# Performance work log

Hardware: AMD Instinct MI355X
Metric: run time of the kernel (lower is better)

Reference implementation:

```python
import jax, jax.numpy as jnp
import numpy as np

A = 64    # number of discrete actions (expert matrices)
D = 512   # input/output feature dim
B = 2048  # batch size


def setup_inputs() -> dict:
    key = jax.random.key(0)
    kx, ka, kw, kb = jax.random.split(key, 4)
    stdv = 1.0 / np.sqrt(D)  # matches torch init: uniform(-stdv, stdv), stdv = 1/sqrt(weight.size(1))
    x = jax.random.normal(kx, (B, D), dtype=jnp.float32)
    a = jax.random.randint(ka, (B,), 0, A, dtype=jnp.int64)
    weight = jax.random.uniform(kw, (A, D, D), dtype=jnp.float32, minval=-stdv, maxval=stdv)
    bias = jax.random.uniform(kb, (A, D), dtype=jnp.float32, minval=-stdv, maxval=stdv)
    return {"x": x, "a": a, "weight": weight, "bias": bias}


def reference(x, a, weight, bias):
    # Per-sample weight gather + batched matvec:
    #   z[b, i] = sum_j weight[a[b], i, j] * x[b, j] + bias[a[b], i]
    w = weight[a]                              # [B, D, D] gathered per-sample matrices
    z = jnp.einsum('bij,bj->bi', w, x)         # batched matvec
    z = z + bias[a]                            # per-sample bias gather + add
    return z
```

## Files before the change

### kernel.cpp

```cpp
#include <hip/hip_runtime.h>


#define NA 64
#define DD 512
#define NB 2048
#define BN 128
#define NW 8
#define BK 64
#define NSTEPS 8

typedef __bf16  bf16x8  __attribute__((ext_vector_type(8)));
typedef __bf16  bf16x4  __attribute__((ext_vector_type(4)));
typedef float   floatx4 __attribute__((ext_vector_type(4)));

#define GLD16(g, l)                                                         \
  __builtin_amdgcn_global_load_lds(                                         \
      (const __attribute__((address_space(1))) void*)(g),                   \
      (__attribute__((address_space(3))) void*)(l), 16, 0, 0)
#define VMCNT(n) asm volatile("s_waitcnt vmcnt(" #n ")" ::: "memory")
#define LGKMCNT0 asm volatile("s_waitcnt lgkmcnt(0)" ::: "memory")
#define SBAR     __builtin_amdgcn_s_barrier()
#define SCHED0   __builtin_amdgcn_sched_barrier(0)

static __device__ inline bf16x8 cvt8(floatx4 lo, floatx4 hi) {
    bf16x8 r;
    r[0] = (__bf16)lo[0]; r[1] = (__bf16)lo[1];
    r[2] = (__bf16)lo[2]; r[3] = (__bf16)lo[3];
    r[4] = (__bf16)hi[0]; r[5] = (__bf16)hi[1];
    r[6] = (__bf16)hi[2]; r[7] = (__bf16)hi[3];
    return r;
}

__global__ __launch_bounds__(512, 1) void dl_fused(
        const float* __restrict__ x,
        const int*   __restrict__ act,
        const float* __restrict__ weight,
        const float* __restrict__ bias,
        float*       __restrict__ out)
{
    const int a    = blockIdx.x;
    const int tid  = threadIdx.x;
    const int wave = tid >> 6;
    const int lane = tid & 63;
    const int l16  = lane & 15;
    const int kgrp = lane >> 4;
    const int colbase = blockIdx.y * BN;
    const int ncol    = colbase + wave * 16 + l16;

    __shared__ int s_perm[NB];
    __shared__ int s_wcnt[NW];
    __shared__ __align__(16) __bf16 Xs[64][DD];
    __shared__ __align__(16) float  Wl[2][BN][BK];

    const float* wtile = weight + (size_t)a * DD * DD + (size_t)colbase * DD;

    const int rr4 = lane >> 4;
    const int u16 = lane & 15;

    auto issue_step = [&](int slot, int s) {
#pragma unroll
        for (int c = 0; c < 4; ++c) {
            const int riw = c * 4 + rr4;
            GLD16(wtile + (size_t)(wave * 16 + riw) * DD + s * BK
                        + ((u16 ^ riw) << 2),
                  (char*)&Wl[slot][wave * 16 + c * 4][0]);
        }
    };

    const int ibase = wave * (NB / NW);
    int myact[NB / NW / 64];
#pragma unroll
    for (int it = 0; it < NB / NW / 64; ++it)
        myact[it] = act[ibase + it * 64 + lane];

    issue_step(0, 0);
    issue_step(1, 1);

    int wcnt = 0;
#pragma unroll
    for (int it = 0; it < NB / NW / 64; ++it) {
        unsigned long long m = __ballot(myact[it] == a);
        wcnt += (int)__popcll(m);
    }
    if (lane == 0) s_wcnt[wave] = wcnt;
    LGKMCNT0; SBAR;
    int cnt = 0, off = 0;
#pragma unroll
    for (int v = 0; v < NW; ++v) {
        const int c = s_wcnt[v];
        if (v < wave) off += c;
        cnt += c;
    }
    if (cnt == 0) { VMCNT(0); return; }
#pragma unroll
    for (int it = 0; it < NB / NW / 64; ++it) {
        unsigned long long m = __ballot(myact[it] == a);
        if (myact[it] == a) {
            int pos = off + (int)__popcll(m & ((1ull << lane) - 1ull));
            s_perm[pos] = ibase + it * 64 + lane;
        }
        off += (int)__popcll(m);
    }
    LGKMCNT0; SBAR;

    const float bias_v = bias[(size_t)a * DD + ncol];
    const int   h      = l16 & 7;
    const int   srow   = tid >> 5;
    const int   skk    = (tid & 31) << 2;

    for (int m0 = 0; m0 < cnt; m0 += 64) {
        if (m0 > 0) { issue_step(0, 0); issue_step(1, 1); }
        const int rem    = min(cnt - m0, 64);
        const int nchunk = (rem + 15) >> 4;

        floatx4 xv[16];
#pragma unroll
        for (int i = 0; i < 4; ++i) {
            const int r  = srow + 16 * i;
            const int rr = (r < rem) ? r : (rem - 1);
            const float* xr = x + (size_t)s_perm[m0 + rr] * DD;
#pragma unroll
            for (int j = 0; j < 4; ++j)
                xv[i * 4 + j] = *(const floatx4*)(xr + skk + 128 * j);
        }

#pragma unroll
        for (int i = 0; i < 4; ++i) {
            const int r = srow + 16 * i;
            if (r < rem) {
                const int rs = (r & 7) << 3;
#pragma unroll
                for (int j = 0; j < 4; ++j) {
                    const int f0 = skk + 128 * j;
                    bf16x4 bv;
#pragma unroll
                    for (int q = 0; q < 4; ++q) bv[q] = (__bf16)xv[i * 4 + j][q];
                    *(bf16x4*)&Xs[r][f0 ^ rs] = bv;
                }
            }
        }
        LGKMCNT0; SBAR;

        floatx4 acc[4] = {{0,0,0,0},{0,0,0,0},{0,0,0,0},{0,0,0,0}};
        const char* wlrow0 = (const char*)&Wl[0][wave * 16 + l16][0];
        const char* wlrow1 = (const char*)&Wl[1][wave * 16 + l16][0];

        auto compute = [&](int slot, int s) {
            const char* wl = slot ? wlrow1 : wlrow0;
#pragma unroll
            for (int s2 = 0; s2 < 2; ++s2) {
                const int u0 = s2 * 8 + kgrp * 2;
                const floatx4 blo = *(const floatx4*)(wl + (((u0)     ^ l16) << 4));
                const floatx4 bhi = *(const floatx4*)(wl + (((u0 + 1) ^ l16) << 4));
                const bf16x8 bfrag = cvt8(blo, bhi);
                const int kb = (s * BK + s2 * 32 + kgrp * 8) ^ (h << 3);
#pragma unroll
                for (int mc = 0; mc < 4; ++mc) {
                    if (mc < nchunk) {
                        const bf16x8 afrag = *(const bf16x8*)&Xs[mc * 16 + l16][kb];
                        acc[mc] = __builtin_amdgcn_mfma_f32_16x16x32_bf16(
                                      afrag, bfrag, acc[mc], 0, 0, 0);
                    }
                }
            }
        };

#pragma unroll
        for (int i = 0; i < NSTEPS; ++i) {
            if (i < NSTEPS - 1) { VMCNT(4); } else { VMCNT(0); }
            SCHED0;
            compute(i & 1, i);
            if (i + 2 < NSTEPS) issue_step(i & 1, i + 2);
        }

#pragma unroll
        for (int mc = 0; mc < 4; ++mc) {
            if (mc < nchunk) {
#pragma unroll
                for (int r = 0; r < 4; ++r) {
                    const int mloc = mc * 16 + kgrp * 4 + r;
                    if (mloc < rem)
                        out[(size_t)s_perm[m0 + mloc] * DD + ncol] =
                            acc[mc][r] + bias_v;
                }
            }
        }
        LGKMCNT0; SBAR;
    }
}

extern "C" void kernel_launch(void* const* d_in, const int* in_sizes, int n_in,
                              void* d_out, int out_size, void* d_ws, size_t ws_size,
                              hipStream_t stream) {
    const float* x      = (const float*)d_in[0];
    const int*   act    = (const int*)  d_in[1];
    const float* weight = (const float*)d_in[2];
    const float* bias   = (const float*)d_in[3];
    float*       out    = (float*)d_out;

    dl_fused<<<dim3(NA, DD / BN), 512, 0, stream>>>(x, act, weight, bias, out);
}
```

Measured before the change: 19.42 us.

## Shrink tiles to 64 columns and 48-row chunks for two blocks per CU

Result: faster. 18.94 us (-2.5%).

```diff
diff --git a/kernel.cpp b/kernel.cpp
--- a/kernel.cpp
+++ b/kernel.cpp
@@ -4,10 +4,11 @@
 #define NA 64
 #define DD 512
 #define NB 2048
-#define BN 128
-#define NW 8
-#define BK 64
-#define NSTEPS 8
+#define BN 64
+#define NW 4
+#define MT 48
+#define BK 32
+#define NSTEPS 16
 
 typedef __bf16  bf16x8  __attribute__((ext_vector_type(8)));
 typedef __bf16  bf16x4  __attribute__((ext_vector_type(4)));
@@ -31,7 +32,7 @@
     return r;
 }
 
-__global__ __launch_bounds__(512, 1) void dl_fused(
+__global__ __launch_bounds__(256, 2) void dl_fused(
         const float* __restrict__ x,
         const int*   __restrict__ act,
         const float* __restrict__ weight,
@@ -44,27 +45,26 @@
     const int lane = tid & 63;
     const int l16  = lane & 15;
     const int kgrp = lane >> 4;
+    const int h    = l16 & 7;
     const int colbase = blockIdx.y * BN;
     const int ncol    = colbase + wave * 16 + l16;
 
-    __shared__ int s_perm[NB];
+    __shared__ __align__(16) __bf16 Xs[MT][DD];
+    __shared__ __align__(16) float  Wl[2][BN][BK];
+    __shared__ unsigned short s_perm[NB];
     __shared__ int s_wcnt[NW];
-    __shared__ __align__(16) __bf16 Xs[64][DD];
-    __shared__ __align__(16) float  Wl[2][BN][BK];
 
     const float* wtile = weight + (size_t)a * DD * DD + (size_t)colbase * DD;
 
-    const int rr4 = lane >> 4;
-    const int u16 = lane & 15;
+    const int r8 = lane >> 3;
+    const int u8 = lane & 7;
 
     auto issue_step = [&](int slot, int s) {
 #pragma unroll
-        for (int c = 0; c < 4; ++c) {
-            const int riw = c * 4 + rr4;
-            GLD16(wtile + (size_t)(wave * 16 + riw) * DD + s * BK
-                        + ((u16 ^ riw) << 2),
-                  (char*)&Wl[slot][wave * 16 + c * 4][0]);
-        }
+        for (int c = 0; c < 2; ++c)
+            GLD16(wtile + (size_t)(wave * 16 + c * 8 + r8) * DD + s * BK
+                        + ((u8 ^ r8) << 2),
+                  (char*)&Wl[slot][wave * 16 + c * 8][0]);
     };
 
     const int ibase = wave * (NB / NW);
@@ -78,10 +78,8 @@
 
     int wcnt = 0;
 #pragma unroll
-    for (int it = 0; it < NB / NW / 64; ++it) {
-        unsigned long long m = __ballot(myact[it] == a);
-        wcnt += (int)__popcll(m);
-    }
+    for (int it = 0; it < NB / NW / 64; ++it)
+        wcnt += (int)__popcll(__ballot(myact[it] == a));
     if (lane == 0) s_wcnt[wave] = wcnt;
     LGKMCNT0; SBAR;
     int cnt = 0, off = 0;
@@ -97,36 +95,34 @@
         unsigned long long m = __ballot(myact[it] == a);
         if (myact[it] == a) {
             int pos = off + (int)__popcll(m & ((1ull << lane) - 1ull));
-            s_perm[pos] = ibase + it * 64 + lane;
+            s_perm[pos] = (unsigned short)(ibase + it * 64 + lane);
         }
         off += (int)__popcll(m);
     }
     LGKMCNT0; SBAR;
 
     const float bias_v = bias[(size_t)a * DD + ncol];
-    const int   h      = l16 & 7;
     const int   srow   = tid >> 5;
     const int   skk    = (tid & 31) << 2;
 
-    for (int m0 = 0; m0 < cnt; m0 += 64) {
+    for (int m0 = 0; m0 < cnt; m0 += MT) {
         if (m0 > 0) { issue_step(0, 0); issue_step(1, 1); }
-        const int rem    = min(cnt - m0, 64);
+        const int rem    = min(cnt - m0, MT);
         const int nchunk = (rem + 15) >> 4;
 
-        floatx4 xv[16];
+        floatx4 xv[24];
 #pragma unroll
-        for (int i = 0; i < 4; ++i) {
-            const int r  = srow + 16 * i;
+        for (int i = 0; i < 6; ++i) {
+            const int r  = srow + 8 * i;
             const int rr = (r < rem) ? r : (rem - 1);
             const float* xr = x + (size_t)s_perm[m0 + rr] * DD;
 #pragma unroll
             for (int j = 0; j < 4; ++j)
                 xv[i * 4 + j] = *(const floatx4*)(xr + skk + 128 * j);
         }
-
 #pragma unroll
-        for (int i = 0; i < 4; ++i) {
-            const int r = srow + 16 * i;
+        for (int i = 0; i < 6; ++i) {
+            const int r = srow + 8 * i;
             if (r < rem) {
                 const int rs = (r & 7) << 3;
 #pragma unroll
@@ -141,40 +137,34 @@
         }
         LGKMCNT0; SBAR;
 
-        floatx4 acc[4] = {{0,0,0,0},{0,0,0,0},{0,0,0,0},{0,0,0,0}};
-        const char* wlrow0 = (const char*)&Wl[0][wave * 16 + l16][0];
-        const char* wlrow1 = (const char*)&Wl[1][wave * 16 + l16][0];
+        floatx4 acc[3] = {{0,0,0,0},{0,0,0,0},{0,0,0,0}};
 
         auto compute = [&](int slot, int s) {
-            const char* wl = slot ? wlrow1 : wlrow0;
+            const char* wl = (const char*)&Wl[slot][wave * 16 + l16][0];
+            const floatx4 blo = *(const floatx4*)(wl + (((2 * kgrp)     ^ h) << 4));
+            const floatx4 bhi = *(const floatx4*)(wl + (((2 * kgrp + 1) ^ h) << 4));
+            const bf16x8 bfrag = cvt8(blo, bhi);
+            const int kb = (s * BK + kgrp * 8) ^ (h << 3);
 #pragma unroll
-            for (int s2 = 0; s2 < 2; ++s2) {
-                const int u0 = s2 * 8 + kgrp * 2;
-                const floatx4 blo = *(const floatx4*)(wl + (((u0)     ^ l16) << 4));
-                const floatx4 bhi = *(const floatx4*)(wl + (((u0 + 1) ^ l16) << 4));
-                const bf16x8 bfrag = cvt8(blo, bhi);
-                const int kb = (s * BK + s2 * 32 + kgrp * 8) ^ (h << 3);
-#pragma unroll
-                for (int mc = 0; mc < 4; ++mc) {
-                    if (mc < nchunk) {
-                        const bf16x8 afrag = *(const bf16x8*)&Xs[mc * 16 + l16][kb];
-                        acc[mc] = __builtin_amdgcn_mfma_f32_16x16x32_bf16(
-                                      afrag, bfrag, acc[mc], 0, 0, 0);
-                    }
+            for (int mc = 0; mc < 3; ++mc) {
+                if (mc < nchunk) {
+                    const bf16x8 afrag = *(const bf16x8*)&Xs[mc * 16 + l16][kb];
+                    acc[mc] = __builtin_amdgcn_mfma_f32_16x16x32_bf16(
+                                  afrag, bfrag, acc[mc], 0, 0, 0);
                 }
             }
         };
 
 #pragma unroll
         for (int i = 0; i < NSTEPS; ++i) {
-            if (i < NSTEPS - 1) { VMCNT(4); } else { VMCNT(0); }
+            if (i < NSTEPS - 1) { VMCNT(2); } else { VMCNT(0); }
             SCHED0;
             compute(i & 1, i);
             if (i + 2 < NSTEPS) issue_step(i & 1, i + 2);
         }
 
 #pragma unroll
-        for (int mc = 0; mc < 4; ++mc) {
+        for (int mc = 0; mc < 3; ++mc) {
             if (mc < nchunk) {
 #pragma unroll
                 for (int r = 0; r < 4; ++r) {
@@ -198,5 +188,5 @@
     const float* bias   = (const float*)d_in[3];
     float*       out    = (float*)d_out;
 
-    dl_fused<<<dim3(NA, DD / BN), 512, 0, stream>>>(x, act, weight, bias, out);
+    dl_fused<<<dim3(NA, DD / BN), 256, 0, stream>>>(x, act, weight, bias, out);
 }
```
